# Performance work log

Measured on AMD Instinct MI355X. Metric: run time of the kernel, lower is better.

## Reference

```python
import jax, jax.numpy as jnp
import numpy as np

N, E, IN, HID, OUT = 40000, 640000, 128, 512, 256


def setup_inputs() -> dict:
    key = jax.random.key(0)
    ks = jax.random.split(key, 8)
    x = jax.random.normal(ks[0], (N, IN), dtype=jnp.float32)
    edge_index = jax.random.randint(ks[1], (2, E), 0, N, dtype=jnp.int64)
    # SAGEConv params: lin_l (applied to aggregated neighbors, with bias),
    # lin_r (applied to root nodes, no bias) -- PyG defaults.
    def lin(k, fin, fout):
        return jax.random.normal(k, (fin, fout), dtype=jnp.float32) / np.sqrt(fin)
    return {
        "x": x,
        "edge_index": edge_index,
        "W1l": lin(ks[2], IN, HID),
        "b1": jnp.zeros((HID,), jnp.float32),
        "W1r": lin(ks[3], IN, HID),
        "W2l": lin(ks[4], HID, OUT),
        "b2": jnp.zeros((OUT,), jnp.float32),
        "W2r": lin(ks[5], HID, OUT),
    }


def _sage_conv(x, src, dst, Wl, b, Wr):
    n = x.shape[0]
    # gather messages from source nodes, mean-aggregate at destination
    msg = x[src]                                            # [E, F]
    agg = jax.ops.segment_sum(msg, dst, num_segments=n)     # [N, F]
    cnt = jax.ops.segment_sum(jnp.ones((src.shape[0],), x.dtype), dst,
                              num_segments=n)               # [N]
    agg = agg / jnp.maximum(cnt, 1.0)[:, None]
    # out = lin_l(mean_neighbors) + lin_r(x)
    return agg @ Wl + b + x @ Wr


def reference(x, edge_index, W1l, b1, W1r, W2l, b2, W2r):
    src, dst = edge_index[0], edge_index[1]
    h = jax.nn.relu(_sage_conv(x, src, dst, W1l, b1, W1r))
    return _sage_conv(h, src, dst, W2l, b2, W2r)
```

## Files before the change

### kernel.cpp

```cpp
#include <hip/hip_runtime.h>


#define N_NODES 40000
#define N_EDGES 640000
#define F_IN 128
#define F_HID 512
#define F_OUT 256
#define NB_SCAN 157

typedef unsigned short ushort_t;
typedef __attribute__((ext_vector_type(8))) short bf16x8;
typedef __attribute__((ext_vector_type(4))) float floatx4;

__device__ __forceinline__ ushort_t f2bf(float f) {
  union { float f; unsigned int u; } x; x.f = f;
  unsigned int r = (x.u + 0x7FFFu + ((x.u >> 16) & 1u)) >> 16;
  return (ushort_t)r;
}
__device__ __forceinline__ float bf2f(ushort_t u) {
  union { unsigned int u; float f; } x; x.u = ((unsigned int)u) << 16;
  return x.f;
}

__global__ void scanA_kernel(const int* __restrict__ deg, int* __restrict__ bsum) {
  __shared__ int sdata[256];
  int i = blockIdx.x * 256 + threadIdx.x;
  sdata[threadIdx.x] = (i < N_NODES) ? deg[i] : 0;
  __syncthreads();
  #pragma unroll
  for (int off = 128; off > 0; off >>= 1) {
    if (threadIdx.x < off) sdata[threadIdx.x] += sdata[threadIdx.x + off];
    __syncthreads();
  }
  if (threadIdx.x == 0) bsum[blockIdx.x] = sdata[0];
}

__global__ void scanB_kernel(const int* __restrict__ bsum, int* __restrict__ boff) {
  __shared__ int buf[2][256];
  int tid = threadIdx.x;
  int v = (tid < NB_SCAN) ? bsum[tid] : 0;
  buf[0][tid] = v;
  __syncthreads();
  int cur = 0;
  #pragma unroll
  for (int off = 1; off < 256; off <<= 1) {
    int val = buf[cur][tid];
    if (tid >= off) val += buf[cur][tid - off];
    buf[cur ^ 1][tid] = val;
    __syncthreads();
    cur ^= 1;
  }
  if (tid < NB_SCAN) boff[tid] = buf[cur][tid] - v;
}

__global__ void scanC_kernel(const int* __restrict__ deg, const int* __restrict__ boff,
                             int* __restrict__ rowptr, int* __restrict__ cursor) {
  __shared__ int buf[2][256];
  int tid = threadIdx.x;
  int i = blockIdx.x * 256 + tid;
  int v = (i < N_NODES) ? deg[i] : 0;
  buf[0][tid] = v;
  __syncthreads();
  int cur = 0;
  #pragma unroll
  for (int off = 1; off < 256; off <<= 1) {
    int val = buf[cur][tid];
    if (tid >= off) val += buf[cur][tid - off];
    buf[cur ^ 1][tid] = val;
    __syncthreads();
    cur ^= 1;
  }
  if (i < N_NODES) {
    int ex = boff[blockIdx.x] + buf[cur][tid] - v;
    rowptr[i] = ex;
    cursor[i] = ex;
    if (i == N_NODES - 1) rowptr[N_NODES] = ex + v;
  }
}

__global__ void fill_kernel(const int* __restrict__ ei, int* __restrict__ cursor,
                            int* __restrict__ col) {
  int e = blockIdx.x * blockDim.x + threadIdx.x;
  if (e < N_EDGES) {
    int d = ei[N_EDGES + e];
    int s = ei[e];
    int pos = atomicAdd(&cursor[d], 1);
    col[pos] = s;
  }
}

__device__ __forceinline__ void wp_body(const float* __restrict__ W,
                                        ushort_t* __restrict__ Wp,
                                        int i, int K, int N, int rowoff, int koff,
                                        int KT) {
  if (i < K * N) {
    int n = i / K, k = i - n * K;
    int ng = rowoff + n, kg = koff + k;
    int gg = ng >> 6, ni = (ng >> 4) & 3, lm = ng & 15;
    int c = kg >> 3, j = kg & 7, t = c >> 2, qk = c & 3;
    size_t dst = (((size_t)(gg * (KT / 32) + t) * 4 + ni) * 64 + qk * 16 + lm) * 8 + j;
    Wp[dst] = f2bf(W[(size_t)k * N + n]);
  }
}

#define PREP_BLOCKS 9038
__global__ void prep_kernel(const float* __restrict__ x, ushort_t* __restrict__ xb,
                            const float* __restrict__ W1l, const float* __restrict__ W1r,
                            const float* __restrict__ W2l, const float* __restrict__ W2r,
                            ushort_t* __restrict__ Wp1, ushort_t* __restrict__ Wp2,
                            const float* __restrict__ b2, float* __restrict__ bc,
                            const int* __restrict__ ei, int* __restrict__ deg) {
  int b = blockIdx.x, tid = threadIdx.x;
  if (b < 5000) {
    int i = b * 256 + tid;
    const int n4 = (N_NODES * F_IN) / 4;
    if (i < n4) {
      float4 v = ((const float4*)x)[i];
      ushort4 o;
      o.x = f2bf(v.x); o.y = f2bf(v.y); o.z = f2bf(v.z); o.w = f2bf(v.w);
      ((ushort4*)xb)[i] = o;
    }
  } else if (b < 5256) {
    wp_body(W1l, Wp1, (b - 5000) * 256 + tid, 128, 512, 0, 0, 256);
  } else if (b < 5512) {
    wp_body(W1r, Wp1, (b - 5256) * 256 + tid, 128, 512, 0, 128, 256);
  } else if (b < 6024) {
    wp_body(W2l, Wp2, (b - 5512) * 256 + tid, 512, 256, 0, 0, 512);
  } else if (b < 6536) {
    wp_body(W2r, Wp2, (b - 6024) * 256 + tid, 512, 256, 256, 0, 512);
  } else if (b < 6538) {
    int i = (b - 6536) * 256 + tid;
    if (i < 512) bc[i] = (i < 256) ? 0.f : b2[i - 256];
  } else {
    int e = (b - 6538) * 256 + tid;
    if (e < N_EDGES) atomicAdd(&deg[ei[N_EDGES + e]], 1);
  }
}

__global__ __launch_bounds__(256) void agg1_kernel(
    const ushort_t* __restrict__ Xb, ushort_t* __restrict__ Yb,
    const int* __restrict__ rowptr, const int* __restrict__ colidx) {
  const int wave = threadIdx.x >> 6, lane = threadIdx.x & 63;
  const int n = blockIdx.x * 4 + wave;
  const int s = rowptr[n], e = rowptr[n + 1];
  float s0 = 0.f, s1 = 0.f;
  for (int base = s; base < e; base += 64) {
    int cnt = min(64, e - base);
    int c = (base + lane < e) ? colidx[base + lane] : 0;
    int j = 0;
    for (; j + 8 <= cnt; j += 8) {
      unsigned int v[8];
      #pragma unroll
      for (int u = 0; u < 8; ++u) {
        int col = __builtin_amdgcn_readlane(c, j + u);
        v[u] = *(const unsigned int*)(Xb + (size_t)col * F_IN + 2 * lane);
      }
      #pragma unroll
      for (int u = 0; u < 8; ++u) {
        s0 += bf2f((ushort_t)(v[u] & 0xffffu));
        s1 += bf2f((ushort_t)(v[u] >> 16));
      }
    }
    for (; j < cnt; ++j) {
      int col = __builtin_amdgcn_readlane(c, j);
      unsigned int v = *(const unsigned int*)(Xb + (size_t)col * F_IN + 2 * lane);
      s0 += bf2f((ushort_t)(v & 0xffffu));
      s1 += bf2f((ushort_t)(v >> 16));
    }
  }
  float inv = 1.f / fmaxf((float)(e - s), 1.f);
  unsigned int o = (unsigned int)f2bf(s0 * inv) | ((unsigned int)f2bf(s1 * inv) << 16);
  *(unsigned int*)(Yb + (size_t)n * F_IN + 2 * lane) = o;
}

__global__ void agg2_kernel(const ushort_t* __restrict__ hl, const float* __restrict__ hr,
                            float* __restrict__ out,
                            const int* __restrict__ rowptr, const int* __restrict__ colidx) {
  __shared__ int cols[128];
  int n = blockIdx.x, f = threadIdx.x;
  int s = rowptr[n], e = rowptr[n + 1];
  float2 hrv = *(const float2*)(hr + (size_t)n * F_OUT + 2 * f);
  float s0 = 0.f, s1 = 0.f;
  for (int base = s; base < e; base += 128) {
    int cnt = min(128, e - base);
    __syncthreads();
    if (f < cnt) cols[f] = colidx[base + f];
    __syncthreads();
    int j = 0;
    for (; j + 8 <= cnt; j += 8) {
      unsigned int v[8];
      #pragma unroll
      for (int u = 0; u < 8; ++u)
        v[u] = *(const unsigned int*)(hl + (size_t)cols[j + u] * F_OUT + 2 * f);
      #pragma unroll
      for (int u = 0; u < 8; ++u) {
        s0 += bf2f((ushort_t)(v[u] & 0xffffu));
        s1 += bf2f((ushort_t)(v[u] >> 16));
      }
    }
    for (; j < cnt; ++j) {
      unsigned int v = *(const unsigned int*)(hl + (size_t)cols[j] * F_OUT + 2 * f);
      s0 += bf2f((ushort_t)(v & 0xffffu));
      s1 += bf2f((ushort_t)(v >> 16));
    }
  }
  float inv = 1.f / fmaxf((float)(e - s), 1.f);
  float2 o;
  o.x = s0 * inv + hrv.x;
  o.y = s1 * inv + hrv.y;
  *(float2*)(out + (size_t)n * F_OUT + 2 * f) = o;
}

template <bool TWOPAIR, bool RELU, bool BIAS, bool OUT_BF16, bool SPLITOUT, int KT>
__global__ __launch_bounds__(512) void gemm_mfma(
    const ushort_t* __restrict__ A0, const ushort_t* __restrict__ A1,
    const ushort_t* __restrict__ Wp, const float* __restrict__ bias,
    float* __restrict__ Cf, ushort_t* __restrict__ Cb, int M) {
  const int NKC = KT / 8;
  __shared__ ushort_t Apan[32 * KT];
  const int tid = threadIdx.x;
  const int wave = tid >> 6, lane = tid & 63;
  const int lm = lane & 15, qk = lane >> 4;
  const int bm = blockIdx.x * 32;
  const int K0 = TWOPAIR ? KT / 2 : KT;
  const int K0c = K0 / 8;

  const ushort_t* wpg = Wp + (size_t)wave * (KT / 32) * 2048;
#define LDB(t, ni) (*(const bf16x8*)(wpg + ((size_t)((t) * 4 + (ni))) * 512 + lane * 8))

  #pragma unroll
  for (int q = 0; q < (32 * NKC) / 512; ++q) {
    int c = tid + q * 512;
    int lc = c & (NKC - 1);
    int row = c / NKC;
    const ushort_t* src = (TWOPAIR && lc >= K0c)
        ? A1 + (size_t)(bm + row) * K0 + (lc - K0c) * 8
        : A0 + (size_t)(bm + row) * K0 + lc * 8;
    bf16x8 v = *(const bf16x8*)src;
    size_t off = ((size_t)(lc * 32 + row) * 16) ^ (size_t)((lc & 7) << 4);
    *(bf16x8*)((char*)Apan + off) = v;
  }

  bf16x8 b00 = LDB(0, 0), b01 = LDB(0, 1), b02 = LDB(0, 2), b03 = LDB(0, 3);
  bf16x8 b04 = LDB(1, 0), b05 = LDB(1, 1), b06 = LDB(1, 2), b07 = LDB(1, 3);
  bf16x8 b10 = LDB(2, 0), b11 = LDB(2, 1), b12 = LDB(2, 2), b13 = LDB(2, 3);
  bf16x8 b14 = LDB(3, 0), b15 = LDB(3, 1), b16 = LDB(3, 2), b17 = LDB(3, 3);
  __syncthreads();

  floatx4 acc[2][4] = {};
#define MM32(k, f0, f1, f2, f3) do {                                        \
    const int kc_ = (k) / 8 + qk;                                           \
    size_t o0_ = ((size_t)(kc_ * 32 + lm) * 16) ^ (size_t)((kc_ & 7) << 4); \
    size_t o1_ = o0_ ^ (16 * 16);                                           \
    bf16x8 av0_ = *(const bf16x8*)((char*)Apan + o0_);                      \
    bf16x8 av1_ = *(const bf16x8*)((char*)Apan + o1_);                      \
    acc[0][0] = __builtin_amdgcn_mfma_f32_16x16x32_bf16(f0, av0_, acc[0][0], 0, 0, 0); \
    acc[0][1] = __builtin_amdgcn_mfma_f32_16x16x32_bf16(f1, av0_, acc[0][1], 0, 0, 0); \
    acc[0][2] = __builtin_amdgcn_mfma_f32_16x16x32_bf16(f2, av0_, acc[0][2], 0, 0, 0); \
    acc[0][3] = __builtin_amdgcn_mfma_f32_16x16x32_bf16(f3, av0_, acc[0][3], 0, 0, 0); \
    acc[1][0] = __builtin_amdgcn_mfma_f32_16x16x32_bf16(f0, av1_, acc[1][0], 0, 0, 0); \
    acc[1][1] = __builtin_amdgcn_mfma_f32_16x16x32_bf16(f1, av1_, acc[1][1], 0, 0, 0); \
    acc[1][2] = __builtin_amdgcn_mfma_f32_16x16x32_bf16(f2, av1_, acc[1][2], 0, 0, 0); \
    acc[1][3] = __builtin_amdgcn_mfma_f32_16x16x32_bf16(f3, av1_, acc[1][3], 0, 0, 0); \
  } while (0)

  #pragma unroll 1
  for (int kb = 0; kb < KT; kb += 128) {
    const int t = kb / 32;
    MM32(kb,      b00, b01, b02, b03);
    MM32(kb + 32, b04, b05, b06, b07);
    if (kb + 128 < KT) {
      b00 = LDB(t + 4, 0); b01 = LDB(t + 4, 1); b02 = LDB(t + 4, 2); b03 = LDB(t + 4, 3);
      b04 = LDB(t + 5, 0); b05 = LDB(t + 5, 1); b06 = LDB(t + 5, 2); b07 = LDB(t + 5, 3);
    }
    MM32(kb + 64, b10, b11, b12, b13);
    MM32(kb + 96, b14, b15, b16, b17);
    if (kb + 192 < KT) {
      b10 = LDB(t + 6, 0); b11 = LDB(t + 6, 1); b12 = LDB(t + 6, 2); b13 = LDB(t + 6, 3);
      b14 = LDB(t + 7, 0); b15 = LDB(t + 7, 1); b16 = LDB(t + 7, 2); b17 = LDB(t + 7, 3);
    }
  }
#undef MM32
#undef LDB

  #pragma unroll
  for (int ni = 0; ni < 4; ++ni) {
    int colg = wave * 64 + ni * 16 + qk * 4;
    float4 b4 = {0.f, 0.f, 0.f, 0.f};
    if (BIAS) b4 = *(const float4*)&bias[colg];
    #pragma unroll
    for (int mi = 0; mi < 2; ++mi) {
      int rowg = bm + mi * 16 + lm;
      float v0 = acc[mi][ni][0] + b4.x;
      float v1 = acc[mi][ni][1] + b4.y;
      float v2 = acc[mi][ni][2] + b4.z;
      float v3 = acc[mi][ni][3] + b4.w;
      if (RELU) {
        v0 = fmaxf(v0, 0.f); v1 = fmaxf(v1, 0.f);
        v2 = fmaxf(v2, 0.f); v3 = fmaxf(v3, 0.f);
      }
      if (SPLITOUT) {
        if (colg < 256) {
          ushort4 o = {f2bf(v0), f2bf(v1), f2bf(v2), f2bf(v3)};
          *(ushort4*)&Cb[(size_t)rowg * 256 + colg] = o;
        } else {
          float4 o = {v0, v1, v2, v3};
          *(float4*)&Cf[(size_t)rowg * 256 + (colg - 256)] = o;
        }
      } else if (OUT_BF16) {
        ushort4 o = {f2bf(v0), f2bf(v1), f2bf(v2), f2bf(v3)};
        *(ushort4*)&Cb[(size_t)rowg * 512 + colg] = o;
      } else {
        float4 o = {v0, v1, v2, v3};
        *(float4*)&Cf[(size_t)rowg * 512 + colg] = o;
      }
    }
  }
}

extern "C" void kernel_launch(void* const* d_in, const int* in_sizes, int n_in,
                              void* d_out, int out_size, void* d_ws, size_t ws_size,
                              hipStream_t stream) {
  const float* x = (const float*)d_in[0];
  const int* ei = (const int*)d_in[1];
  const float* W1l = (const float*)d_in[2];
  const float* b1 = (const float*)d_in[3];
  const float* W1r = (const float*)d_in[4];
  const float* W2l = (const float*)d_in[5];
  const float* b2 = (const float*)d_in[6];
  const float* W2r = (const float*)d_in[7];
  float* out = (float*)d_out;

  char* ws = (char*)d_ws;
  size_t off = 0;
  auto alloc = [&](size_t bytes) {
    void* p = ws + off;
    off = (off + bytes + 255) & ~(size_t)255;
    return p;
  };
  int* deg = (int*)alloc((size_t)N_NODES * 4);
  int* rowptr = (int*)alloc((size_t)(N_NODES + 1) * 4);
  int* cursor = (int*)alloc((size_t)N_NODES * 4);
  int* col = (int*)alloc((size_t)N_EDGES * 4);
  int* bsum = (int*)alloc((size_t)NB_SCAN * 4);
  int* boff = (int*)alloc((size_t)NB_SCAN * 4);
  ushort_t* x_bf = (ushort_t*)alloc((size_t)N_NODES * F_IN * 2);
  ushort_t* aggx_bf = (ushort_t*)alloc((size_t)N_NODES * F_IN * 2);
  ushort_t* h_bf = (ushort_t*)alloc((size_t)N_NODES * F_HID * 2);
  ushort_t* hl_bf = (ushort_t*)alloc((size_t)N_NODES * F_OUT * 2);
  float* hr = (float*)alloc((size_t)N_NODES * F_OUT * 4);
  ushort_t* Wp1 = (ushort_t*)alloc((size_t)512 * 256 * 2);
  ushort_t* Wp2 = (ushort_t*)alloc((size_t)512 * 512 * 2);
  float* biascat = (float*)alloc(512 * 4);

  hipMemsetAsync(deg, 0, (size_t)N_NODES * 4, stream);
  prep_kernel<<<PREP_BLOCKS, 256, 0, stream>>>(
      x, x_bf, W1l, W1r, W2l, W2r, Wp1, Wp2, b2, biascat, ei, deg);

  scanA_kernel<<<NB_SCAN, 256, 0, stream>>>(deg, bsum);
  scanB_kernel<<<1, 256, 0, stream>>>(bsum, boff);
  scanC_kernel<<<NB_SCAN, 256, 0, stream>>>(deg, boff, rowptr, cursor);
  fill_kernel<<<(N_EDGES + 255) / 256, 256, 0, stream>>>(ei, cursor, col);

  agg1_kernel<<<N_NODES / 4, 256, 0, stream>>>(x_bf, aggx_bf, rowptr, col);
  gemm_mfma<true, true, true, true, false, 256>
      <<<1250, 512, 0, stream>>>(
          aggx_bf, x_bf, Wp1, b1, nullptr, h_bf, N_NODES);

  gemm_mfma<false, false, true, false, true, 512>
      <<<1250, 512, 0, stream>>>(
          h_bf, nullptr, Wp2, biascat, hr, hl_bf, N_NODES);
  agg2_kernel<<<N_NODES, 128, 0, stream>>>(hl_bf, hr, out, rowptr, col);
}
```

Measured before the change: 297.0 us.

## Fuse layer-1 and layer-2 GEMMs keeping hidden activations in LDS

Merges the two MFMA GEMM kernels into one. The ReLU'd bf16 hidden tile (32x512) is written to a swizzled shared-memory panel and consumed directly by the second GEMM, so the h_bf round trip through global memory (about 40 MB of traffic) and one kernel launch go away. The B-operand prefetch is also reworked from a 4-deep register set to a 2-deep ping-pong, which lowers register pressure but gives less latency hiding. LDS use per block rises to 48 KB, which may reduce occupancy.

```diff
diff --git a/kernel.cpp b/kernel.cpp
--- a/kernel.cpp
+++ b/kernel.cpp
@@ -211,108 +211,131 @@
   *(float2*)(out + (size_t)n * F_OUT + 2 * f) = o;
 }
 
-template <bool TWOPAIR, bool RELU, bool BIAS, bool OUT_BF16, bool SPLITOUT, int KT>
-__global__ __launch_bounds__(512) void gemm_mfma(
-    const ushort_t* __restrict__ A0, const ushort_t* __restrict__ A1,
-    const ushort_t* __restrict__ Wp, const float* __restrict__ bias,
-    float* __restrict__ Cf, ushort_t* __restrict__ Cb, int M) {
-  const int NKC = KT / 8;
-  __shared__ ushort_t Apan[32 * KT];
+__device__ __forceinline__ void mm32(const ushort_t* Apan, int k, int qk, int lm,
+                                     bf16x8 f0, bf16x8 f1, bf16x8 f2, bf16x8 f3,
+                                     floatx4 (&acc)[2][4]) {
+  const int kc = k / 8 + qk;
+  size_t o0 = ((size_t)(kc * 32 + lm) * 16) ^ (size_t)((kc & 7) << 4);
+  bf16x8 av0 = *(const bf16x8*)((const char*)Apan + o0);
+  bf16x8 av1 = *(const bf16x8*)((const char*)Apan + (o0 ^ 256));
+  acc[0][0] = __builtin_amdgcn_mfma_f32_16x16x32_bf16(f0, av0, acc[0][0], 0, 0, 0);
+  acc[0][1] = __builtin_amdgcn_mfma_f32_16x16x32_bf16(f1, av0, acc[0][1], 0, 0, 0);
+  acc[0][2] = __builtin_amdgcn_mfma_f32_16x16x32_bf16(f2, av0, acc[0][2], 0, 0, 0);
+  acc[0][3] = __builtin_amdgcn_mfma_f32_16x16x32_bf16(f3, av0, acc[0][3], 0, 0, 0);
+  acc[1][0] = __builtin_amdgcn_mfma_f32_16x16x32_bf16(f0, av1, acc[1][0], 0, 0, 0);
+  acc[1][1] = __builtin_amdgcn_mfma_f32_16x16x32_bf16(f1, av1, acc[1][1], 0, 0, 0);
+  acc[1][2] = __builtin_amdgcn_mfma_f32_16x16x32_bf16(f2, av1, acc[1][2], 0, 0, 0);
+  acc[1][3] = __builtin_amdgcn_mfma_f32_16x16x32_bf16(f3, av1, acc[1][3], 0, 0, 0);
+}
+
+__global__ __launch_bounds__(512) void gemm_fused(
+    const ushort_t* __restrict__ A0,
+    const ushort_t* __restrict__ A1,
+    const ushort_t* __restrict__ Wp1,
+    const float* __restrict__ b1,
+    const ushort_t* __restrict__ Wp2,
+    const float* __restrict__ bc,
+    float* __restrict__ hr, ushort_t* __restrict__ hl) {
+  __shared__ ushort_t Apan[32 * 256];
+  __shared__ ushort_t Hpan[32 * 512];
   const int tid = threadIdx.x;
   const int wave = tid >> 6, lane = tid & 63;
   const int lm = lane & 15, qk = lane >> 4;
   const int bm = blockIdx.x * 32;
-  const int K0 = TWOPAIR ? KT / 2 : KT;
-  const int K0c = K0 / 8;
-
-  const ushort_t* wpg = Wp + (size_t)wave * (KT / 32) * 2048;
-#define LDB(t, ni) (*(const bf16x8*)(wpg + ((size_t)((t) * 4 + (ni))) * 512 + lane * 8))
-
-  #pragma unroll
-  for (int q = 0; q < (32 * NKC) / 512; ++q) {
+
+  const ushort_t* wpg1 = Wp1 + (size_t)wave * 8 * 2048;
+  const ushort_t* wpg2 = Wp2 + (size_t)wave * 16 * 2048;
+#define LDB1(t, ni) (*(const bf16x8*)(wpg1 + ((size_t)(t) * 4 + (ni)) * 512 + lane * 8))
+#define LDB2(t, ni) (*(const bf16x8*)(wpg2 + ((size_t)(t) * 4 + (ni)) * 512 + lane * 8))
+
+  #pragma unroll
+  for (int q = 0; q < 2; ++q) {
     int c = tid + q * 512;
-    int lc = c & (NKC - 1);
-    int row = c / NKC;
-    const ushort_t* src = (TWOPAIR && lc >= K0c)
-        ? A1 + (size_t)(bm + row) * K0 + (lc - K0c) * 8
-        : A0 + (size_t)(bm + row) * K0 + lc * 8;
+    int lc = c & 31;
+    int row = c >> 5;
+    const ushort_t* src = (lc >= 16)
+        ? A1 + (size_t)(bm + row) * 128 + (lc - 16) * 8
+        : A0 + (size_t)(bm + row) * 128 + lc * 8;
     bf16x8 v = *(const bf16x8*)src;
     size_t off = ((size_t)(lc * 32 + row) * 16) ^ (size_t)((lc & 7) << 4);
     *(bf16x8*)((char*)Apan + off) = v;
   }
 
-  bf16x8 b00 = LDB(0, 0), b01 = LDB(0, 1), b02 = LDB(0, 2), b03 = LDB(0, 3);
-  bf16x8 b04 = LDB(1, 0), b05 = LDB(1, 1), b06 = LDB(1, 2), b07 = LDB(1, 3);
-  bf16x8 b10 = LDB(2, 0), b11 = LDB(2, 1), b12 = LDB(2, 2), b13 = LDB(2, 3);
-  bf16x8 b14 = LDB(3, 0), b15 = LDB(3, 1), b16 = LDB(3, 2), b17 = LDB(3, 3);
-  __syncthreads();
-
-  floatx4 acc[2][4] = {};
-#define MM32(k, f0, f1, f2, f3) do {                                        \
-    const int kc_ = (k) / 8 + qk;                                           \
-    size_t o0_ = ((size_t)(kc_ * 32 + lm) * 16) ^ (size_t)((kc_ & 7) << 4); \
-    size_t o1_ = o0_ ^ (16 * 16);                                           \
-    bf16x8 av0_ = *(const bf16x8*)((char*)Apan + o0_);                      \
-    bf16x8 av1_ = *(const bf16x8*)((char*)Apan + o1_);                      \
-    acc[0][0] = __builtin_amdgcn_mfma_f32_16x16x32_bf16(f0, av0_, acc[0][0], 0, 0, 0); \
-    acc[0][1] = __builtin_amdgcn_mfma_f32_16x16x32_bf16(f1, av0_, acc[0][1], 0, 0, 0); \
-    acc[0][2] = __builtin_amdgcn_mfma_f32_16x16x32_bf16(f2, av0_, acc[0][2], 0, 0, 0); \
-    acc[0][3] = __builtin_amdgcn_mfma_f32_16x16x32_bf16(f3, av0_, acc[0][3], 0, 0, 0); \
-    acc[1][0] = __builtin_amdgcn_mfma_f32_16x16x32_bf16(f0, av1_, acc[1][0], 0, 0, 0); \
-    acc[1][1] = __builtin_amdgcn_mfma_f32_16x16x32_bf16(f1, av1_, acc[1][1], 0, 0, 0); \
-    acc[1][2] = __builtin_amdgcn_mfma_f32_16x16x32_bf16(f2, av1_, acc[1][2], 0, 0, 0); \
-    acc[1][3] = __builtin_amdgcn_mfma_f32_16x16x32_bf16(f3, av1_, acc[1][3], 0, 0, 0); \
-  } while (0)
-
+  bf16x8 bvA[4], bvB[4];
+  #pragma unroll
+  for (int ni = 0; ni < 4; ++ni) bvA[ni] = LDB1(0, ni);
+  __syncthreads();
+
+  floatx4 acc1[2][4] = {};
   #pragma unroll 1
-  for (int kb = 0; kb < KT; kb += 128) {
-    const int t = kb / 32;
-    MM32(kb,      b00, b01, b02, b03);
-    MM32(kb + 32, b04, b05, b06, b07);
-    if (kb + 128 < KT) {
-      b00 = LDB(t + 4, 0); b01 = LDB(t + 4, 1); b02 = LDB(t + 4, 2); b03 = LDB(t + 4, 3);
-      b04 = LDB(t + 5, 0); b05 = LDB(t + 5, 1); b06 = LDB(t + 5, 2); b07 = LDB(t + 5, 3);
-    }
-    MM32(kb + 64, b10, b11, b12, b13);
-    MM32(kb + 96, b14, b15, b16, b17);
-    if (kb + 192 < KT) {
-      b10 = LDB(t + 6, 0); b11 = LDB(t + 6, 1); b12 = LDB(t + 6, 2); b13 = LDB(t + 6, 3);
-      b14 = LDB(t + 7, 0); b15 = LDB(t + 7, 1); b16 = LDB(t + 7, 2); b17 = LDB(t + 7, 3);
-    }
-  }
-#undef MM32
-#undef LDB
+  for (int kb = 0; kb < 256; kb += 64) {
+    const int t0 = kb / 32;
+    #pragma unroll
+    for (int ni = 0; ni < 4; ++ni) bvB[ni] = LDB1(t0 + 1, ni);
+    mm32(Apan, kb, qk, lm, bvA[0], bvA[1], bvA[2], bvA[3], acc1);
+    if (kb + 64 < 256) {
+      #pragma unroll
+      for (int ni = 0; ni < 4; ++ni) bvA[ni] = LDB1(t0 + 2, ni);
+    }
+    mm32(Apan, kb + 32, qk, lm, bvB[0], bvB[1], bvB[2], bvB[3], acc1);
+  }
 
   #pragma unroll
   for (int ni = 0; ni < 4; ++ni) {
     int colg = wave * 64 + ni * 16 + qk * 4;
-    float4 b4 = {0.f, 0.f, 0.f, 0.f};
-    if (BIAS) b4 = *(const float4*)&bias[colg];
+    float4 b4 = *(const float4*)&b1[colg];
+    int lc2 = colg >> 3;
+    int sub = (qk & 1) * 8;
+    #pragma unroll
+    for (int mi = 0; mi < 2; ++mi) {
+      int row = mi * 16 + lm;
+      ushort4 o;
+      o.x = f2bf(fmaxf(acc1[mi][ni][0] + b4.x, 0.f));
+      o.y = f2bf(fmaxf(acc1[mi][ni][1] + b4.y, 0.f));
+      o.z = f2bf(fmaxf(acc1[mi][ni][2] + b4.z, 0.f));
+      o.w = f2bf(fmaxf(acc1[mi][ni][3] + b4.w, 0.f));
+      size_t off = (((size_t)(lc2 * 32 + row) * 16) ^ (size_t)((lc2 & 7) << 4)) + sub;
+      *(ushort4*)((char*)Hpan + off) = o;
+    }
+  }
+
+  #pragma unroll
+  for (int ni = 0; ni < 4; ++ni) bvA[ni] = LDB2(0, ni);
+  __syncthreads();
+
+  floatx4 acc2[2][4] = {};
+  #pragma unroll 1
+  for (int kb = 0; kb < 512; kb += 64) {
+    const int t0 = kb / 32;
+    #pragma unroll
+    for (int ni = 0; ni < 4; ++ni) bvB[ni] = LDB2(t0 + 1, ni);
+    mm32(Hpan, kb, qk, lm, bvA[0], bvA[1], bvA[2], bvA[3], acc2);
+    if (kb + 64 < 512) {
+      #pragma unroll
+      for (int ni = 0; ni < 4; ++ni) bvA[ni] = LDB2(t0 + 2, ni);
+    }
+    mm32(Hpan, kb + 32, qk, lm, bvB[0], bvB[1], bvB[2], bvB[3], acc2);
+  }
+#undef LDB1
+#undef LDB2
+
+  #pragma unroll
+  for (int ni = 0; ni < 4; ++ni) {
+    int colg = wave * 64 + ni * 16 + qk * 4;
+    float4 b4 = *(const float4*)&bc[colg];
     #pragma unroll
     for (int mi = 0; mi < 2; ++mi) {
       int rowg = bm + mi * 16 + lm;
-      float v0 = acc[mi][ni][0] + b4.x;
-      float v1 = acc[mi][ni][1] + b4.y;
-      float v2 = acc[mi][ni][2] + b4.z;
-      float v3 = acc[mi][ni][3] + b4.w;
-      if (RELU) {
-        v0 = fmaxf(v0, 0.f); v1 = fmaxf(v1, 0.f);
-        v2 = fmaxf(v2, 0.f); v3 = fmaxf(v3, 0.f);
-      }
-      if (SPLITOUT) {
-        if (colg < 256) {
-          ushort4 o = {f2bf(v0), f2bf(v1), f2bf(v2), f2bf(v3)};
-          *(ushort4*)&Cb[(size_t)rowg * 256 + colg] = o;
-        } else {
-          float4 o = {v0, v1, v2, v3};
-          *(float4*)&Cf[(size_t)rowg * 256 + (colg - 256)] = o;
-        }
-      } else if (OUT_BF16) {
+      float v0 = acc2[mi][ni][0] + b4.x;
+      float v1 = acc2[mi][ni][1] + b4.y;
+      float v2 = acc2[mi][ni][2] + b4.z;
+      float v3 = acc2[mi][ni][3] + b4.w;
+      if (colg < 256) {
         ushort4 o = {f2bf(v0), f2bf(v1), f2bf(v2), f2bf(v3)};
-        *(ushort4*)&Cb[(size_t)rowg * 512 + colg] = o;
+        *(ushort4*)&hl[(size_t)rowg * 256 + colg] = o;
       } else {
         float4 o = {v0, v1, v2, v3};
-        *(float4*)&Cf[(size_t)rowg * 512 + colg] = o;
+        *(float4*)&hr[(size_t)rowg * 256 + (colg - 256)] = o;
       }
     }
   }
@@ -346,7 +369,6 @@
   int* boff = (int*)alloc((size_t)NB_SCAN * 4);
   ushort_t* x_bf = (ushort_t*)alloc((size_t)N_NODES * F_IN * 2);
   ushort_t* aggx_bf = (ushort_t*)alloc((size_t)N_NODES * F_IN * 2);
-  ushort_t* h_bf = (ushort_t*)alloc((size_t)N_NODES * F_HID * 2);
   ushort_t* hl_bf = (ushort_t*)alloc((size_t)N_NODES * F_OUT * 2);
   float* hr = (float*)alloc((size_t)N_NODES * F_OUT * 4);
   ushort_t* Wp1 = (ushort_t*)alloc((size_t)512 * 256 * 2);
@@ -363,12 +385,7 @@
   fill_kernel<<<(N_EDGES + 255) / 256, 256, 0, stream>>>(ei, cursor, col);
 
   agg1_kernel<<<N_NODES / 4, 256, 0, stream>>>(x_bf, aggx_bf, rowptr, col);
-  gemm_mfma<true, true, true, true, false, 256>
-      <<<1250, 512, 0, stream>>>(
-          aggx_bf, x_bf, Wp1, b1, nullptr, h_bf, N_NODES);
-
-  gemm_mfma<false, false, true, false, true, 512>
-      <<<1250, 512, 0, stream>>>(
-          h_bf, nullptr, Wp2, biascat, hr, hl_bf, N_NODES);
+  gemm_fused<<<1250, 512, 0, stream>>>(
+      aggx_bf, x_bf, Wp1, b1, Wp2, biascat, hr, hl_bf);
   agg2_kernel<<<N_NODES, 128, 0, stream>>>(hl_bf, hr, out, rowptr, col);
 }
```

Measured after the change: 281.7 us. 1.05x faster.
